# Performance work log

Measured on AMD Instinct MI355X. Metric: run time of the kernel, lower is better.

The kernel has to match this reference:

```python
import jax, jax.numpy as jnp
import numpy as np

B, V = 256, 128000


def setup_inputs() -> dict:
    key = jax.random.key(0)
    k1, k2 = jax.random.split(key)
    logits = jax.random.normal(k1, (B, V), dtype=jnp.float32) * 4.0
    # temperatures in [0.3, 1.2] to avoid division by ~0
    temperatures = jax.random.uniform(k2, (B,), dtype=jnp.float32) * 0.9 + 0.3
    return {"logits": logits, "temperatures": temperatures}


def reference(logits, temperatures):
    # temperature-scaled softmax
    x = logits.astype(jnp.float32) / temperatures[:, None]
    probs = jax.nn.softmax(x, axis=-1)  # (B, V)
    # torch.empty_like(probs).exponential_(1).clamp_min_(1e-10)
    noise = jnp.maximum(
        jax.random.exponential(jax.random.key(42), probs.shape, dtype=jnp.float32),
        1e-10,
    )
    # Gumbel-max style sampling: argmax of probs / Exp(1) noise
    return jnp.argmax(probs / noise, axis=-1)  # (B,) int
```

## Files before the change

### kernel.cpp

```cpp
#include <hip/hip_runtime.h>
#include <stdint.h>
#include <math.h>

#define BB 256
#define ROW 128000
#define SPLITM 32
#define CHUNKM (ROW / SPLITM)
#define GRIDM (BB * SPLITM)
#define THREADS 512
#define WAVES (THREADS / 64)

#define SEED_THREADS 256
#define SEED_STRIDE 496

#define TF_K2 0x1BD11BF0u
#define SMALL_BITS 0x00100000u
#define MIN_L 1.4426950408889634e-10f
#define LN2 0.69314718055994530942f
#define GMAX 33.0f
#define MODE_CNT_THR 1152

__device__ __forceinline__ uint32_t rotl32(uint32_t x, int r) {
    return __builtin_amdgcn_alignbit(x, x, 32 - r);
}

#define R1S(r)        { x0 += x1; x1 = rotl32(x1, (r)) ^ x0; }
#define RI1S(r, A, B) { x1 += (B); x0 = x0 + (A) + x1; x1 = rotl32(x1, (r)) ^ x0; }

__device__ __forceinline__ uint32_t threefry1_xor(uint32_t c) {
    uint32_t x1 = c + 42u;
    uint32_t x0 = x1;
    x1 = rotl32(x1, 13) ^ x0;
    R1S(15) R1S(26) R1S(6)
    RI1S(17, 42u, TF_K2 + 1u)
    R1S(29) R1S(16) R1S(24)
    RI1S(13, TF_K2, 2u)
    R1S(15) R1S(26) R1S(6)
    RI1S(17, 0u, 45u)
    R1S(29) R1S(16) R1S(24)
    RI1S(13, 42u, TF_K2 + 4u)
    R1S(15) R1S(26) R1S(6)
    return (x0 + TF_K2) ^ (x1 + 5u);
}

__device__ __forceinline__ void threefry8_xor(uint32_t c, uint32_t bits[8]) {
    uint32_t x0[8], x1[8];
#pragma unroll
    for (int j = 0; j < 8; ++j) x1[j] = c + (uint32_t)(j + 42);
#pragma unroll
    for (int j = 0; j < 8; ++j) { x0[j] = x1[j]; x1[j] = rotl32(x1[j], 13) ^ x0[j]; }

#define RND(r)                                        \
    do { _Pragma("unroll")                            \
        for (int j = 0; j < 8; ++j) {                 \
            x0[j] += x1[j];                           \
            x1[j] = rotl32(x1[j], (r)) ^ x0[j];       \
        } } while (0)
#define RNDI(r, A, B)                                 \
    do { _Pragma("unroll")                            \
        for (int j = 0; j < 8; ++j) {                 \
            x1[j] += (B);                             \
            x0[j] = x0[j] + (A) + x1[j];              \
            x1[j] = rotl32(x1[j], (r)) ^ x0[j];       \
        } } while (0)

    RND(15); RND(26); RND(6);
    RNDI(17, 42u, TF_K2 + 1u);
    RND(29); RND(16); RND(24);
    RNDI(13, TF_K2, 2u);
    RND(15); RND(26); RND(6);
    RNDI(17, 0u, 45u);
    RND(29); RND(16); RND(24);
    RNDI(13, 42u, TF_K2 + 4u);
    RND(15); RND(26); RND(6);
#undef RND
#undef RNDI

#pragma unroll
    for (int j = 0; j < 8; ++j) bits[j] = (x0[j] + TF_K2) ^ (x1[j] + 5u);
}

__device__ __forceinline__ float noise_negL(uint32_t bits) {
    const float uf = __uint_as_float(0x3F800000u | (bits >> 9));
    const float L = __builtin_amdgcn_logf(2.0f - uf);
    const float u = uf - 1.0f;
    const float es2 = u * fmaf(u, fmaf(u, fmaf(u,
        -0.3606737602222408f, -0.4808983469629878f),
        -0.7213475204444817f), -1.4426950408889634f);
    const float es2c = fminf(es2, -MIN_L);
    return (bits < SMALL_BITS) ? es2c : L;
}

__device__ __forceinline__ float score1(float x, float invT2, uint32_t bits) {
    const float L = noise_negL(bits);
    return fmaf(x, invT2, -__builtin_amdgcn_logf(-L));
}

__device__ __forceinline__ uint32_t f2o(float f) {
    uint32_t u = __float_as_uint(f);
    return (u & 0x80000000u) ? ~u : (u | 0x80000000u);
}

__global__ __launch_bounds__(THREADS) void chunkmax_kernel(
    const float* __restrict__ logits, float* __restrict__ cmx,
    uint32_t* __restrict__ cmi) {
    const int g = blockIdx.x;
    const int b = g >> 5, q = g & 31;
    const float* rowp = logits + (size_t)b * ROW + (size_t)q * CHUNKM;
    const int tid = threadIdx.x;
    const int rel = tid * 8;

    float mx = -INFINITY;
    uint32_t mi = 0u;
    if (rel < CHUNKM) {
        const float4 xa = *reinterpret_cast<const float4*>(rowp + rel);
        const float4 xb = *reinterpret_cast<const float4*>(rowp + rel + 4);
        const float xs[8] = {xa.x, xa.y, xa.z, xa.w, xb.x, xb.y, xb.z, xb.w};
#pragma unroll
        for (int j = 0; j < 8; ++j)
            if (xs[j] > mx) { mx = xs[j]; mi = (uint32_t)(rel + j); }
    }
#pragma unroll
    for (int off = 32; off >= 1; off >>= 1) {
        const float ox = __shfl_xor(mx, off);
        const uint32_t oi = __shfl_xor(mi, off);
        if (ox > mx) { mx = ox; mi = oi; }
    }
    __shared__ float smx[WAVES];
    __shared__ uint32_t smi[WAVES];
    const int lane = tid & 63, wid = tid >> 6;
    if (lane == 0) { smx[wid] = mx; smi[wid] = mi; }
    __syncthreads();
    if (tid == 0) {
        mx = smx[0]; mi = smi[0];
#pragma unroll
        for (int w = 1; w < WAVES; ++w)
            if (smx[w] > mx) { mx = smx[w]; mi = smi[w]; }
        cmx[g] = mx;
        cmi[g] = (uint32_t)(q * CHUNKM) + mi;
    }
}

__global__ __launch_bounds__(SEED_THREADS) void rowseed_kernel(
    const float* __restrict__ logits, const float* __restrict__ temps,
    const float* __restrict__ cmx, const uint32_t* __restrict__ cmi,
    float* __restrict__ gs, int* __restrict__ mode) {
    const int b = blockIdx.x;
    const int t = threadIdx.x;
    const float T = temps[b];
    const float invT2 = 1.0f / (T * LN2);
    const int off = t * SEED_STRIDE;
    const float* rowp = logits + (size_t)b * ROW + off;
    const uint32_t cb = (uint32_t)b * ROW + (uint32_t)off;

    const float4 xa = *reinterpret_cast<const float4*>(rowp);
    const float4 xb = *reinterpret_cast<const float4*>(rowp + 4);
    const float xs[8] = {xa.x, xa.y, xa.z, xa.w, xb.x, xb.y, xb.z, xb.w};
    uint32_t bits[8];
    threefry8_xor(cb, bits);

    float bs = -INFINITY;
#pragma unroll
    for (int j = 0; j < 8; ++j) bs = fmaxf(bs, score1(xs[j], invT2, bits[j]));

    if (t < SPLITM) {
        const uint32_t idx = cmi[b * SPLITM + t];
        const float xm = cmx[b * SPLITM + t];
        bs = fmaxf(bs, score1(xm, invT2,
                              threefry1_xor((uint32_t)b * ROW + idx)));
    }

#pragma unroll
    for (int o = 32; o >= 1; o >>= 1) bs = fmaxf(bs, __shfl_xor(bs, o));
    __shared__ float sred[SEED_THREADS / 64];
    __shared__ int scr[SEED_THREADS / 64];
    const int lane = t & 63, wid = t >> 6;
    if (lane == 0) sred[wid] = bs;
    __syncthreads();
    const float gsv = fmaxf(fmaxf(sred[0], sred[1]), fmaxf(sred[2], sred[3]));

    const float xthr = (gsv - GMAX) * (T * LN2);
    int c = 0;
#pragma unroll
    for (int j = 0; j < 8; ++j) c += (xs[j] > xthr) ? 1 : 0;
#pragma unroll
    for (int o = 32; o >= 1; o >>= 1) c += __shfl_xor(c, o);
    if (lane == 0) scr[wid] = c;
    __syncthreads();
    if (t == 0) {
        const int tot = scr[0] + scr[1] + scr[2] + scr[3];
        gs[b] = gsv;
        mode[b] = (tot > MODE_CNT_THR) ? 1 : 0;
    }
}

__global__ __launch_bounds__(THREADS, 4) void sampler_kernel(
    const float* __restrict__ logits, const float* __restrict__ temps,
    const float* __restrict__ gs, const int* __restrict__ mode,
    unsigned long long* __restrict__ parts) {
    __shared__ int scnt;
    __shared__ unsigned short qidx[CHUNKM];
    __shared__ unsigned long long sbest[WAVES];

    const int g = blockIdx.x;
    const int b = g >> 5, q = g & 31;
    const float T = temps[b];
    const float invT2 = 1.0f / (T * LN2);
    const float xthr = (gs[b] - GMAX) * (T * LN2);
    const float* rowp = logits + (size_t)b * ROW + (size_t)q * CHUNKM;
    const uint32_t cbase = (uint32_t)b * ROW + (uint32_t)(q * CHUNKM);
    const int tid = threadIdx.x;
    const int lane = tid & 63;
    const unsigned long long lmask_lt = (1ull << lane) - 1ull;

    if (tid == 0) scnt = 0;
    __syncthreads();

    const int rel = tid * 8;
    const bool act = rel < CHUNKM;
    float xs[8];
    if (act) {
        const float4 xa = *reinterpret_cast<const float4*>(rowp + rel);
        const float4 xb = *reinterpret_cast<const float4*>(rowp + rel + 4);
        xs[0]=xa.x; xs[1]=xa.y; xs[2]=xa.z; xs[3]=xa.w;
        xs[4]=xb.x; xs[5]=xb.y; xs[6]=xb.z; xs[7]=xb.w;
    }

    float best_s = -INFINITY;
    uint32_t best_rel = 0u;

    if (mode[b]) {
        if (act) {
            uint32_t bits[8];
            threefry8_xor(cbase + (uint32_t)rel, bits);
            float L8[8];
#pragma unroll
            for (int j = 0; j < 8; ++j) {
                const float uf = __uint_as_float(0x3F800000u | (bits[j] >> 9));
                L8[j] = __builtin_amdgcn_logf(2.0f - uf);
            }
            const uint32_t b01 = min(min(bits[0], bits[1]), bits[2]);
            const uint32_t b34 = min(min(bits[3], bits[4]), bits[5]);
            const uint32_t b67 = min(bits[6], bits[7]);
            if (__any(min(min(b01, b34), b67) < SMALL_BITS)) {
#pragma unroll
                for (int j = 0; j < 8; ++j) {
                    const float u = __uint_as_float(0x3F800000u |
                                    (bits[j] >> 9)) - 1.0f;
                    const float es2 = u * fmaf(u, fmaf(u, fmaf(u,
                        -0.3606737602222408f, -0.4808983469629878f),
                        -0.7213475204444817f), -1.4426950408889634f);
                    const float es2c = fminf(es2, -MIN_L);
                    L8[j] = (bits[j] < SMALL_BITS) ? es2c : L8[j];
                }
            }
#pragma unroll
            for (int j = 0; j < 8; ++j) {
                const float s = fmaf(xs[j], invT2,
                                     -__builtin_amdgcn_logf(-L8[j]));
                if (s > best_s) { best_s = s; best_rel = (uint32_t)(rel + j); }
            }
        }
    } else {
        if (act) {
#pragma unroll
            for (int j = 0; j < 8; ++j) {
                const bool pass = xs[j] > xthr;
                const unsigned long long mk = __ballot(pass);
                if (mk != 0ull) {
                    int base = 0;
                    if (lane == 0) base = atomicAdd(&scnt, __popcll(mk));
                    base = __builtin_amdgcn_readfirstlane(base);
                    if (pass) {
                        const int pos = base + (int)__popcll(mk & lmask_lt);
                        qidx[pos] = (unsigned short)(rel + j);
                    }
                }
            }
        }
        __syncthreads();
        const int total = scnt;
        for (int i = tid; i < total; i += THREADS) {
            const int r2 = (int)qidx[i];
            const float x = rowp[r2];
            const float s = score1(x, invT2, threefry1_xor(cbase + (uint32_t)r2));
            if (s > best_s) { best_s = s; best_rel = (uint32_t)r2; }
        }
    }

    const uint32_t best_v = (uint32_t)(q * CHUNKM) + best_rel;
    unsigned long long best =
        ((unsigned long long)f2o(best_s) << 32) | (uint32_t)(~best_v);
#pragma unroll
    for (int off = 32; off >= 1; off >>= 1) {
        const unsigned long long o = __shfl_xor(best, off);
        best = (o > best) ? o : best;
    }
    const int wid = tid >> 6;
    if (lane == 0) sbest[wid] = best;
    __syncthreads();
    if (tid == 0) {
        unsigned long long r = sbest[0];
#pragma unroll
        for (int w = 1; w < WAVES; ++w) r = (sbest[w] > r) ? sbest[w] : r;
        parts[g] = r;
    }
}

__global__ __launch_bounds__(BB) void combine_kernel(
    const unsigned long long* __restrict__ parts, int* __restrict__ out) {
    const int b = threadIdx.x;
    const unsigned long long* p = parts + b * SPLITM;
    unsigned long long r = p[0];
#pragma unroll
    for (int w = 1; w < SPLITM; ++w) r = (p[w] > r) ? p[w] : r;
    out[b] = (int)(~(uint32_t)(r & 0xFFFFFFFFull));
}

extern "C" void kernel_launch(void* const* d_in, const int* in_sizes, int n_in,
                              void* d_out, int out_size, void* d_ws, size_t ws_size,
                              hipStream_t stream) {
    const float* logits = (const float*)d_in[0];
    const float* temps = (const float*)d_in[1];
    int* out = (int*)d_out;
    float* cmx = (float*)d_ws;
    uint32_t* cmi = (uint32_t*)((char*)d_ws + 32768);
    float* gs = (float*)((char*)d_ws + 65536);
    int* mode = (int*)((char*)d_ws + 66560);
    unsigned long long* parts =
        (unsigned long long*)((char*)d_ws + 67584);

    hipLaunchKernelGGL(chunkmax_kernel, dim3(GRIDM), dim3(THREADS), 0, stream,
                       logits, cmx, cmi);
    hipLaunchKernelGGL(rowseed_kernel, dim3(BB), dim3(SEED_THREADS), 0, stream,
                       logits, temps, cmx, cmi, gs, mode);
    hipLaunchKernelGGL(sampler_kernel, dim3(GRIDM), dim3(THREADS), 0, stream,
                       logits, temps, gs, mode, parts);
    hipLaunchKernelGGL(combine_kernel, dim3(1), dim3(BB), 0, stream, parts, out);
}
```

Before: 81.13 us.

## Decide row mode before chunkmax and skip chunk-max pass for dense rows

A new premode kernel runs first: it computes a sampled score seed and the dense/sparse mode from strided samples only. The chunkmax kernel then exits early for dense-mode rows, so those rows skip a full read of the logits. The chunk-max candidates are folded into the sparse threshold inside the sampler prologue instead of in a separate rowseed kernel. The mode threshold is raised to rebalance which rows take the full-compute path. The trade-off is that the mode decision now rests on a weaker seed that excludes the chunk maxima.

```diff
diff --git a/kernel.cpp b/kernel.cpp
--- a/kernel.cpp
+++ b/kernel.cpp
@@ -18,7 +18,7 @@
 #define MIN_L 1.4426950408889634e-10f
 #define LN2 0.69314718055994530942f
 #define GMAX 33.0f
-#define MODE_CNT_THR 1152
+#define MODE_CNT_THR 1434
 
 __device__ __forceinline__ uint32_t rotl32(uint32_t x, int r) {
     return __builtin_amdgcn_alignbit(x, x, 32 - r);
@@ -101,11 +101,57 @@
     return (u & 0x80000000u) ? ~u : (u | 0x80000000u);
 }
 
+__global__ __launch_bounds__(SEED_THREADS) void premode_kernel(
+    const float* __restrict__ logits, const float* __restrict__ temps,
+    float* __restrict__ gs0, int* __restrict__ mode) {
+    const int b = blockIdx.x;
+    const int t = threadIdx.x;
+    const float T = temps[b];
+    const float invT2 = 1.0f / (T * LN2);
+    const int off = t * SEED_STRIDE;
+    const float* rowp = logits + (size_t)b * ROW + off;
+    const uint32_t cb = (uint32_t)b * ROW + (uint32_t)off;
+
+    const float4 xa = *reinterpret_cast<const float4*>(rowp);
+    const float4 xb = *reinterpret_cast<const float4*>(rowp + 4);
+    const float xs[8] = {xa.x, xa.y, xa.z, xa.w, xb.x, xb.y, xb.z, xb.w};
+    uint32_t bits[8];
+    threefry8_xor(cb, bits);
+
+    float bs = -INFINITY;
+#pragma unroll
+    for (int j = 0; j < 8; ++j) bs = fmaxf(bs, score1(xs[j], invT2, bits[j]));
+
+#pragma unroll
+    for (int o = 32; o >= 1; o >>= 1) bs = fmaxf(bs, __shfl_xor(bs, o));
+    __shared__ float sred[SEED_THREADS / 64];
+    __shared__ int scr[SEED_THREADS / 64];
+    const int lane = t & 63, wid = t >> 6;
+    if (lane == 0) sred[wid] = bs;
+    __syncthreads();
+    const float gsv = fmaxf(fmaxf(sred[0], sred[1]), fmaxf(sred[2], sred[3]));
+
+    const float xthr = (gsv - GMAX) * (T * LN2);
+    int c = 0;
+#pragma unroll
+    for (int j = 0; j < 8; ++j) c += (xs[j] > xthr) ? 1 : 0;
+#pragma unroll
+    for (int o = 32; o >= 1; o >>= 1) c += __shfl_xor(c, o);
+    if (lane == 0) scr[wid] = c;
+    __syncthreads();
+    if (t == 0) {
+        const int tot = scr[0] + scr[1] + scr[2] + scr[3];
+        gs0[b] = gsv;
+        mode[b] = (tot > MODE_CNT_THR) ? 1 : 0;
+    }
+}
+
 __global__ __launch_bounds__(THREADS) void chunkmax_kernel(
-    const float* __restrict__ logits, float* __restrict__ cmx,
-    uint32_t* __restrict__ cmi) {
+    const float* __restrict__ logits, const int* __restrict__ mode,
+    float* __restrict__ cmx, uint32_t* __restrict__ cmi) {
     const int g = blockIdx.x;
     const int b = g >> 5, q = g & 31;
+    if (mode[b]) return;
     const float* rowp = logits + (size_t)b * ROW + (size_t)q * CHUNKM;
     const int tid = threadIdx.x;
     const int rel = tid * 8;
@@ -141,80 +187,42 @@
     }
 }
 
-__global__ __launch_bounds__(SEED_THREADS) void rowseed_kernel(
+__global__ __launch_bounds__(THREADS, 4) void sampler_kernel(
     const float* __restrict__ logits, const float* __restrict__ temps,
+    const float* __restrict__ gs0, const int* __restrict__ mode,
     const float* __restrict__ cmx, const uint32_t* __restrict__ cmi,
-    float* __restrict__ gs, int* __restrict__ mode) {
-    const int b = blockIdx.x;
-    const int t = threadIdx.x;
+    unsigned long long* __restrict__ parts) {
+    __shared__ int scnt;
+    __shared__ float s_xthr;
+    __shared__ unsigned short qidx[CHUNKM];
+    __shared__ unsigned long long sbest[WAVES];
+
+    const int g = blockIdx.x;
+    const int b = g >> 5, q = g & 31;
+    const int md = mode[b];
     const float T = temps[b];
     const float invT2 = 1.0f / (T * LN2);
-    const int off = t * SEED_STRIDE;
-    const float* rowp = logits + (size_t)b * ROW + off;
-    const uint32_t cb = (uint32_t)b * ROW + (uint32_t)off;
-
-    const float4 xa = *reinterpret_cast<const float4*>(rowp);
-    const float4 xb = *reinterpret_cast<const float4*>(rowp + 4);
-    const float xs[8] = {xa.x, xa.y, xa.z, xa.w, xb.x, xb.y, xb.z, xb.w};
-    uint32_t bits[8];
-    threefry8_xor(cb, bits);
-
-    float bs = -INFINITY;
-#pragma unroll
-    for (int j = 0; j < 8; ++j) bs = fmaxf(bs, score1(xs[j], invT2, bits[j]));
-
-    if (t < SPLITM) {
-        const uint32_t idx = cmi[b * SPLITM + t];
-        const float xm = cmx[b * SPLITM + t];
-        bs = fmaxf(bs, score1(xm, invT2,
-                              threefry1_xor((uint32_t)b * ROW + idx)));
-    }
-
-#pragma unroll
-    for (int o = 32; o >= 1; o >>= 1) bs = fmaxf(bs, __shfl_xor(bs, o));
-    __shared__ float sred[SEED_THREADS / 64];
-    __shared__ int scr[SEED_THREADS / 64];
-    const int lane = t & 63, wid = t >> 6;
-    if (lane == 0) sred[wid] = bs;
-    __syncthreads();
-    const float gsv = fmaxf(fmaxf(sred[0], sred[1]), fmaxf(sred[2], sred[3]));
-
-    const float xthr = (gsv - GMAX) * (T * LN2);
-    int c = 0;
-#pragma unroll
-    for (int j = 0; j < 8; ++j) c += (xs[j] > xthr) ? 1 : 0;
-#pragma unroll
-    for (int o = 32; o >= 1; o >>= 1) c += __shfl_xor(c, o);
-    if (lane == 0) scr[wid] = c;
-    __syncthreads();
-    if (t == 0) {
-        const int tot = scr[0] + scr[1] + scr[2] + scr[3];
-        gs[b] = gsv;
-        mode[b] = (tot > MODE_CNT_THR) ? 1 : 0;
-    }
-}
-
-__global__ __launch_bounds__(THREADS, 4) void sampler_kernel(
-    const float* __restrict__ logits, const float* __restrict__ temps,
-    const float* __restrict__ gs, const int* __restrict__ mode,
-    unsigned long long* __restrict__ parts) {
-    __shared__ int scnt;
-    __shared__ unsigned short qidx[CHUNKM];
-    __shared__ unsigned long long sbest[WAVES];
-
-    const int g = blockIdx.x;
-    const int b = g >> 5, q = g & 31;
-    const float T = temps[b];
-    const float invT2 = 1.0f / (T * LN2);
-    const float xthr = (gs[b] - GMAX) * (T * LN2);
     const float* rowp = logits + (size_t)b * ROW + (size_t)q * CHUNKM;
     const uint32_t cbase = (uint32_t)b * ROW + (uint32_t)(q * CHUNKM);
     const int tid = threadIdx.x;
     const int lane = tid & 63;
     const unsigned long long lmask_lt = (1ull << lane) - 1ull;
 
-    if (tid == 0) scnt = 0;
-    __syncthreads();
+    if (!md) {
+        if (tid == 0) scnt = 0;
+        if (tid < SPLITM) {
+            const uint32_t idx = cmi[b * SPLITM + tid];
+            const float xm = cmx[b * SPLITM + tid];
+            float cs = score1(xm, invT2,
+                              threefry1_xor((uint32_t)b * ROW + idx));
+            cs = fmaxf(cs, gs0[b]);
+#pragma unroll
+            for (int o = 16; o >= 1; o >>= 1)
+                cs = fmaxf(cs, __shfl_xor(cs, o));
+            if (tid == 0) s_xthr = (cs - GMAX) * (T * LN2);
+        }
+        __syncthreads();
+    }
 
     const int rel = tid * 8;
     const bool act = rel < CHUNKM;
@@ -229,7 +237,7 @@
     float best_s = -INFINITY;
     uint32_t best_rel = 0u;
 
-    if (mode[b]) {
+    if (md) {
         if (act) {
             uint32_t bits[8];
             threefry8_xor(cbase + (uint32_t)rel, bits);
@@ -262,6 +270,7 @@
             }
         }
     } else {
+        const float xthr = s_xthr;
         if (act) {
 #pragma unroll
             for (int j = 0; j < 8; ++j) {
@@ -325,16 +334,16 @@
     int* out = (int*)d_out;
     float* cmx = (float*)d_ws;
     uint32_t* cmi = (uint32_t*)((char*)d_ws + 32768);
-    float* gs = (float*)((char*)d_ws + 65536);
+    float* gs0 = (float*)((char*)d_ws + 65536);
     int* mode = (int*)((char*)d_ws + 66560);
     unsigned long long* parts =
         (unsigned long long*)((char*)d_ws + 67584);
 
+    hipLaunchKernelGGL(premode_kernel, dim3(BB), dim3(SEED_THREADS), 0, stream,
+                       logits, temps, gs0, mode);
     hipLaunchKernelGGL(chunkmax_kernel, dim3(GRIDM), dim3(THREADS), 0, stream,
-                       logits, cmx, cmi);
-    hipLaunchKernelGGL(rowseed_kernel, dim3(BB), dim3(SEED_THREADS), 0, stream,
-                       logits, temps, cmx, cmi, gs, mode);
+                       logits, mode, cmx, cmi);
     hipLaunchKernelGGL(sampler_kernel, dim3(GRIDM), dim3(THREADS), 0, stream,
-                       logits, temps, gs, mode, parts);
+                       logits, temps, gs0, mode, cmx, cmi, parts);
     hipLaunchKernelGGL(combine_kernel, dim3(1), dim3(BB), 0, stream, parts, out);
 }
```

Measured after the change: 77.45 us. 4.5% less time.
